# Performance work log

Hardware: AMD Instinct MI355X
Metric: run time of the kernel (lower is better)

## Reference

```python
import math
import jax, jax.numpy as jnp
import numpy as np

L, B, D, Z, H, N = 2048, 8, 1024, 128, 2048, 16
MAXPOS = 2048
LAPLACE_MU, LAPLACE_SIGMA = 0.707107, 0.282095


def setup_inputs() -> dict:
    key = jax.random.key(0)
    ks = jax.random.split(key, 14)
    def rn(k, shp, s=1.0):
        return jax.random.normal(k, shp, dtype=jnp.float32) * s
    return {
        "x": rn(ks[0], (L, B, D)),
        # MultiHeadEMA params (unidirectional: kernel_dim == D)
        "delta": rn(ks[1], (D, N, 1), 0.2),
        "alpha": rn(ks[2], (D, N, 1), 0.2),
        "beta_ema": rn(ks[3], (D, N, 1), 0.02) + 1.0,
        "gamma_ema": rn(ks[4], (D, N)),
        "omega": rn(ks[5], (D,)),
        # projections
        "v_w": rn(ks[6], (D, H), 0.02), "v_b": jnp.zeros((H,), jnp.float32),
        "mx_w": rn(ks[7], (D, Z + H + 2 * D), 0.02),
        "mx_b": jnp.zeros((Z + H + 2 * D,), jnp.float32),
        "h_w": rn(ks[8], (H, D), 0.02), "h_b": jnp.zeros((D,), jnp.float32),
        # q/k affine from shared z
        "qk_gamma": rn(ks[9], (2, Z), 0.1) + 1.0,
        "qk_beta": rn(ks[10], (2, Z), 0.1),
        # simple relative positional bias
        "rel_pos": rn(ks[11], (2 * MAXPOS - 1,), 0.02),
        # prenorm layernorm
        "ln_w": jnp.ones((D,), jnp.float32),
        "ln_b": jnp.zeros((D,), jnp.float32),
    }


def _laplace(x):
    x = (x - LAPLACE_MU) / (LAPLACE_SIGMA * math.sqrt(2.0))
    return 0.5 * (1.0 + jax.lax.erf(x))


def _layer_norm(x, w, b, eps=1e-5):
    mu = jnp.mean(x, axis=-1, keepdims=True)
    var = jnp.mean(jnp.square(x - mu), axis=-1, keepdims=True)
    return (x - mu) * jax.lax.rsqrt(var + eps) * w + b


def _rel_bias(rel_pos, seq_len):
    # SimpleRelativePositionalBias: Toeplitz (L, L) matrix from a 2L-1 vector
    bvec = rel_pos[MAXPOS - seq_len:MAXPOS + seq_len - 1]  # (2L-1,)
    t = jnp.pad(bvec, (0, seq_len))                         # (3L-1,)
    t = jnp.tile(t, seq_len)[:-seq_len].reshape(seq_len, 3 * seq_len - 2)
    r = (2 * seq_len - 1) // 2
    return t[:, r:t.shape[1] - r]                           # (L, L)


def _ema_conv(xn, delta, alpha, beta_ema, gamma_ema, omega, seq_len):
    # xn: (L, B, D) -> silu(EMA(xn) + xn * omega), via FFT convolution
    scale = 1.0 / math.sqrt(N)
    p = jax.nn.sigmoid(delta)                 # (D, N, 1)
    q = 1.0 - p * jax.nn.sigmoid(alpha)       # (D, N, 1)
    vander = jnp.arange(seq_len, dtype=jnp.float32)[None, None, :] * jnp.log(q)  # (D, N, L)
    kernel = jnp.einsum('dnl,dn->dl', p * beta_ema * jnp.exp(vander), gamma_ema * scale)  # (D, L)
    residual = xn * omega                     # (L, B, D)
    xt = jnp.transpose(xn, (1, 2, 0))         # (B, D, L)
    nfft = 2 * seq_len
    kf = jnp.fft.rfft(kernel, n=nfft)         # (D, L+1) complex
    xf = jnp.fft.rfft(xt, n=nfft)             # (B, D, L+1)
    out = jnp.fft.irfft(xf * kf, n=nfft)[..., :seq_len]  # (B, D, L)
    return jax.nn.silu(jnp.transpose(out, (2, 0, 1)) + residual)  # (L, B, D)


def reference(x, delta, alpha, beta_ema, gamma_ema, omega,
              v_w, v_b, mx_w, mx_b, h_w, h_b,
              qk_gamma, qk_beta, rel_pos, ln_w, ln_b):
    seq_len = x.shape[0]
    residual = x
    xn = _layer_norm(x, ln_w, ln_b)                       # prenorm
    v = jax.nn.silu(xn @ v_w + v_b)                        # (L, B, H)
    mx = _ema_conv(xn, delta, alpha, beta_ema, gamma_ema, omega, seq_len)  # (L, B, D)
    base = mx @ mx_w + mx_b                                # (L, B, D+Z+H+D)
    u = jax.nn.sigmoid(base[..., :D])                      # update gate (L, B, D)
    zr = jax.nn.silu(base[..., D:D + Z + H])
    hx = base[..., D + Z + H:]                             # (L, B, D)
    z = zr[..., :Z]                                        # (L, B, Z)
    r = zr[..., Z:]                                        # (L, B, H)
    zqk = z[..., None, :] * qk_gamma + qk_beta             # (L, B, 2, Z)
    q = jnp.transpose(zqk[..., 0, :], (1, 0, 2))           # (B, L, Z)
    k = jnp.transpose(zqk[..., 1, :], (1, 0, 2))           # (B, L, Z)
    vb = jnp.transpose(v, (1, 0, 2))                       # (B, L, H)
    bias = _rel_bias(rel_pos, seq_len)                     # (L, L)
    qk = jnp.einsum('blz,bmz->blm', q, k) / seq_len + bias # (B, L, L)
    attn = _laplace(qk)
    h = jnp.einsum('blm,bmh->blh', attn, vb)               # (B, L, H)
    h = jnp.transpose(h, (1, 0, 2))                        # (L, B, H)
    h = jax.nn.silu(hx + (h * r) @ h_w + h_b)              # (L, B, D)
    out = residual + u * (h - residual)
    return out
```

## Files before the change

kernel.cpp:

```cpp
#include <hip/hip_runtime.h>
#include <hip/hip_bf16.h>
#include <math.h>

typedef unsigned short u16;
typedef unsigned int   u32;
typedef __bf16 bf16x8_t __attribute__((ext_vector_type(8)));
typedef float  f32x4_t  __attribute__((ext_vector_type(4)));

#define DEVI static __device__ __forceinline__

DEVI float bf2f(u16 u){ union{u32 i; float f;} v; v.i = ((u32)u)<<16; return v.f; }
DEVI u16 f2bf(float f){ union{float f; u32 i;} v; v.f = f; u32 i = v.i; i += 0x7fffu + ((i>>16)&1u); return (u16)(i>>16); }
DEVI float sigm(float x){ return 1.0f/(1.0f + __expf(-x)); }
DEVI float silu_(float x){ return x * sigm(x); }

DEVI void gload16(const u16* gsrc, u16* lds){
  __builtin_amdgcn_global_load_lds(
      (const __attribute__((address_space(1))) unsigned int*)gsrc,
      (__attribute__((address_space(3))) unsigned int*)lds, 16, 0, 0);
}

constexpr int L_=2048, B_=8, D_=1024, Z_=128, H_=2048, N_=16;
constexpr int CH_=128, NC_=16;
constexpr int MXN_=4224;

__global__ __launch_bounds__(256) void k_ln(const float* __restrict__ x,
                                            const float* __restrict__ w,
                                            const float* __restrict__ b,
                                            u16* __restrict__ xn){
  int row = blockIdx.x, t = threadIdx.x;
  int l = row >> 3, bb = row & 7;
  const float4* xr = (const float4*)(x + (size_t)row*D_);
  float4 v = xr[t];
  float s  = v.x+v.y+v.z+v.w;
  float sq = v.x*v.x+v.y*v.y+v.z*v.z+v.w*v.w;
  #pragma unroll
  for (int m=1; m<64; m<<=1){ s += __shfl_xor(s, m); sq += __shfl_xor(sq, m); }
  __shared__ float ss[4], sv[4];
  int wv = t>>6;
  if ((t&63)==0){ ss[wv]=s; sv[wv]=sq; }
  __syncthreads();
  s = ss[0]+ss[1]+ss[2]+ss[3]; sq = sv[0]+sv[1]+sv[2]+sv[3];
  float mu = s*(1.0f/D_);
  float var = sq*(1.0f/D_) - mu*mu;
  float rs = rsqrtf(var + 1e-5f);
  float4 wv4 = ((const float4*)w)[t];
  float4 bv4 = ((const float4*)b)[t];
  u16 o0 = f2bf((v.x-mu)*rs*wv4.x+bv4.x);
  u16 o1 = f2bf((v.y-mu)*rs*wv4.y+bv4.y);
  u16 o2 = f2bf((v.z-mu)*rs*wv4.z+bv4.z);
  u16 o3 = f2bf((v.w-mu)*rs*wv4.w+bv4.w);
  *(uint2*)(xn + ((size_t)bb*L_ + l)*D_ + t*4) =
      make_uint2((u32)o0 | ((u32)o1<<16), (u32)o2 | ((u32)o3<<16));
}

__global__ __launch_bounds__(256) void k_tr(const float* __restrict__ in, int R, int C,
                                            u16* __restrict__ out){
  __shared__ u16 TT[32*33];
  int c0 = blockIdx.x*32, r0 = blockIdx.y*32;
  int t = threadIdx.x;
  int lr = t>>3, lc4 = (t&7)*4;
  float4 v = *(const float4*)&in[(size_t)(r0+lr)*C + c0 + lc4];
  TT[(lc4+0)*33 + lr] = f2bf(v.x);
  TT[(lc4+1)*33 + lr] = f2bf(v.y);
  TT[(lc4+2)*33 + lr] = f2bf(v.z);
  TT[(lc4+3)*33 + lr] = f2bf(v.w);
  __syncthreads();
  int orr = t>>3, oc4 = (t&7)*4;
  u16 a0 = TT[orr*33 + oc4+0], a1 = TT[orr*33 + oc4+1];
  u16 a2 = TT[orr*33 + oc4+2], a3 = TT[orr*33 + oc4+3];
  *(uint2*)&out[(size_t)(c0+orr)*R + r0 + oc4] =
      make_uint2((u32)a0 | ((u32)a1<<16), (u32)a2 | ((u32)a3<<16));
}

__global__ void k_ema_params(const float* __restrict__ delta, const float* __restrict__ alpha,
                             const float* __restrict__ beta,  const float* __restrict__ gamma,
                             float* __restrict__ qA, float* __restrict__ wcA, float* __restrict__ qPA){
  int i = blockIdx.x*256 + threadIdx.x;
  if (i >= D_*N_) return;
  float p = 1.0f/(1.0f + expf(-delta[i]));
  float q = 1.0f - p*(1.0f/(1.0f + expf(-alpha[i])));
  qA[i]  = q;
  wcA[i] = p*beta[i]*gamma[i]*0.25f;
  qPA[i] = powf(q, (float)CH_);
}

__global__ __launch_bounds__(256) void k_ema_a(const u16* __restrict__ xn,
                                               const float* __restrict__ qA,
                                               float* __restrict__ F){
  int d = blockIdx.x*256 + threadIdx.x;
  int b = blockIdx.y, c = blockIdx.z;
  float q[N_], s[N_];
  #pragma unroll
  for (int n=0;n<N_;n++){ q[n]=qA[d*N_+n]; s[n]=0.0f; }
  for (int t=0;t<CH_;t++){
    int l = c*CH_ + t;
    float x = bf2f(xn[((size_t)b*L_ + l)*D_ + d]);
    #pragma unroll
    for (int n=0;n<N_;n++) s[n] = q[n]*s[n] + x;
  }
  float* Fo = F + (((size_t)c*B_ + b)*D_ + d)*N_;
  #pragma unroll
  for (int n=0;n<N_;n++) Fo[n] = s[n];
}

__global__ __launch_bounds__(256) void k_ema_b(float* __restrict__ F,
                                               const float* __restrict__ qPA){
  int i = blockIdx.x*256 + threadIdx.x;
  int n = i & (N_-1);
  int d = (i>>4) & (D_-1);
  int b = i >> 14;
  float qP = qPA[d*N_+n];
  float S = 0.0f;
  for (int c=0;c<NC_;c++){
    size_t idx = (((size_t)c*B_ + b)*D_ + d)*N_ + n;
    float f = F[idx];
    F[idx] = S;
    S = qP*S + f;
  }
}

__global__ __launch_bounds__(256) void k_ema_c(const u16* __restrict__ xn,
                                               const float* __restrict__ qA,
                                               const float* __restrict__ wcA,
                                               const float* __restrict__ CY,
                                               const float* __restrict__ omega,
                                               u16* __restrict__ mx){
  int d = blockIdx.x*256 + threadIdx.x;
  int b = blockIdx.y, c = blockIdx.z;
  float q[N_], wc[N_], s[N_];
  const float* cy = CY + (((size_t)c*B_ + b)*D_ + d)*N_;
  #pragma unroll
  for (int n=0;n<N_;n++){ q[n]=qA[d*N_+n]; wc[n]=wcA[d*N_+n]; s[n]=cy[n]; }
  float om = omega[d];
  for (int t=0;t<CH_;t++){
    int l = c*CH_ + t;
    float x = bf2f(xn[((size_t)b*L_ + l)*D_ + d]);
    float acc = 0.0f;
    #pragma unroll
    for (int n=0;n<N_;n++){ s[n] = q[n]*s[n] + x; acc += wc[n]*s[n]; }
    mx[((size_t)b*L_ + l)*D_ + d] = f2bf(silu_(acc + x*om));
  }
}

#define STG(BUF, K0) do {                                                         \
    int _ab = (BUF)*8192;                                                         \
    _Pragma("unroll")                                                             \
    for (int it=0; it<2; ++it){                                                   \
      int idx = it*256 + tid; int r = idx>>2, ch = idx&3;                         \
      gload16(Ab + (size_t)(rowBase + r)*lda + (K0) + ((ch ^ (r&3))*8),           \
              &LDS[_ab + idx*8]);                                                 \
    }                                                                             \
    _Pragma("unroll")                                                             \
    for (int it=0; it<2; ++it){                                                   \
      int idx = it*256 + tid; int r = idx>>2, ch = idx&3;                         \
      gload16(Bb + (size_t)(colBase + r)*ldb + (K0) + ((ch ^ (r&3))*8),           \
              &LDS[_ab + 4096 + idx*8]);                                          \
    }                                                                             \
  } while(0)

#define CMP(BUF) do {                                                             \
    int _ab = (BUF)*8192;                                                         \
    bf16x8_t af[4], bfr[4];                                                       \
    int kfx = (lane4*8) ^ ((lane15&3)<<3);                                        \
    _Pragma("unroll")                                                             \
    for (int m=0;m<4;m++)                                                         \
      af[m]  = *(const bf16x8_t*)&LDS[_ab + (wm + m*16 + lane15)*32 + kfx];       \
    _Pragma("unroll")                                                             \
    for (int n=0;n<4;n++)                                                         \
      bfr[n] = *(const bf16x8_t*)&LDS[_ab + 4096 + (wn + n*16 + lane15)*32 + kfx];\
    __builtin_amdgcn_s_setprio(1);                                                \
    _Pragma("unroll")                                                             \
    for (int m=0;m<4;m++)                                                         \
      _Pragma("unroll")                                                           \
      for (int n=0;n<4;n++)                                                       \
        acc[m][n] = __builtin_amdgcn_mfma_f32_16x16x32_bf16(af[m], bfr[n], acc[m][n], 0,0,0); \
    __builtin_amdgcn_s_setprio(0);                                                \
  } while(0)

template<int OP>
__global__ __launch_bounds__(256) void k_gall(
    const u16* __restrict__ A, int lda, long aStr,
    const u16* __restrict__ Bm, int ldb, long bStr,
    int K,
    u16* __restrict__ C, int ldc, long cStr,
    const float* __restrict__ biasC, const float* __restrict__ biasR,
    const float* __restrict__ relpos,
    const float* __restrict__ qkg, const float* __restrict__ qkb,
    u16* __restrict__ P0, u16* __restrict__ P1,
    u16* __restrict__ P2, u16* __restrict__ P3,
    const u16* __restrict__ RP0, const u16* __restrict__ RP1,
    const float* __restrict__ xin, float* __restrict__ outf, int bb)
{
  __shared__ u16 LDS[16384];
  int zz = blockIdx.z;
  const u16* Ab = A + (size_t)zz*aStr;
  const u16* Bb = Bm + (size_t)zz*bStr;

  int gx = gridDim.x;
  int f = blockIdx.x + gx*blockIdx.y;
  int q8 = (gx*gridDim.y) >> 3;
  int wg = (f & 7)*q8 + (f >> 3);
  int rowBase = (wg / gx)*128;
  int colBase = (wg % gx)*128;

  int tid = threadIdx.x;
  int lane = tid & 63, wave = tid >> 6;
  int wm = (wave>>1)*64, wn = (wave&1)*64;
  int lane15 = lane & 15, lane4 = lane >> 4;

  f32x4_t acc[4][4];
  #pragma unroll
  for (int m=0;m<4;m++)
    #pragma unroll
    for (int n=0;n<4;n++) acc[m][n] = (f32x4_t){0.f,0.f,0.f,0.f};

  int nt = K >> 5;
  STG(0, 0);
  STG(1, 32);
  for (int t = 0; t < nt; ++t){
    if (t + 1 < nt) { asm volatile("s_waitcnt vmcnt(4)" ::: "memory"); }
    else            { asm volatile("s_waitcnt vmcnt(0)" ::: "memory"); }
    __builtin_amdgcn_s_barrier();
    __builtin_amdgcn_sched_barrier(0);
    CMP(t & 1);
    if (t + 2 < nt) {
      __builtin_amdgcn_s_barrier();
      STG(t & 1, (t+2)*32);
    }
  }

  u16* Cb  = C  ? C  + (size_t)zz*cStr : nullptr;
  u16* P0b = P0 ? P0 + (size_t)zz*((size_t)L_*D_) : nullptr;
  u16* P1b = P1 ? P1 + (size_t)zz*((size_t)L_*D_) : nullptr;
  u16* P2b = P2 ? P2 + (size_t)zz*((size_t)L_*Z_) : nullptr;
  u16* P3b = P3 ? P3 + (size_t)zz*((size_t)L_*Z_) : nullptr;
  const u16* RP0b = RP0 ? RP0 + (size_t)zz*(OP==3 ? (size_t)L_*H_ : (size_t)L_*D_) : nullptr;
  const u16* RP1b = RP1 ? RP1 + (size_t)zz*((size_t)L_*D_) : nullptr;
  int bglob = bb + zz;

  #pragma unroll
  for (int m=0;m<4;m++) {
    #pragma unroll
    for (int n=0;n<4;n++) {
      int col = colBase + wn + n*16 + lane15;
      #pragma unroll
      for (int r2=0;r2<4;r2++) {
        int row = rowBase + wm + m*16 + lane4*4 + r2;
        float v = acc[m][n][r2];
        if (OP == 0) {
          Cb[(size_t)row*ldc + col] = f2bf(silu_(v + biasR[row]));
        } else if (OP == 1) {
          v += biasC[col];
          if (col < 1024) {
            P0b[(size_t)row*1024 + col] = f2bf(sigm(v));
          } else if (col < 1152) {
            float s = silu_(v);
            int zi = col - 1024;
            P2b[(size_t)row*128 + zi] = f2bf(s*qkg[zi]     + qkb[zi]);
            P3b[(size_t)row*128 + zi] = f2bf(s*qkg[128+zi] + qkb[128+zi]);
          } else if (col < 3200) {
            Cb[(size_t)row*2048 + (col-1152)] = f2bf(silu_(v));
          } else {
            P1b[(size_t)row*1024 + (col-3200)] = f2bf(v);
          }
        } else if (OP == 2) {
          v = v*(1.0f/(float)L_) + relpos[2047 + col - row];
          v = 0.5f*(1.0f + erff((v - 0.707107f)*2.5066282746f));
          Cb[(size_t)row*ldc + col] = f2bf(v);
        } else if (OP == 3) {
          v *= bf2f(RP0b[(size_t)row*ldc + col]);
          Cb[(size_t)row*ldc + col] = f2bf(v);
        } else {
          v += biasC[col];
          float hx = bf2f(RP0b[(size_t)row*1024 + col]);
          float hval = silu_(hx + v);
          size_t gi = ((size_t)row*B_ + bglob)*D_ + col;
          float xv = xin[gi];
          float uu = bf2f(RP1b[(size_t)row*1024 + col]);
          outf[gi] = xv + uu*(hval - xv);
        }
      }
    }
  }
}

extern "C" void kernel_launch(void* const* d_in, const int* in_sizes, int n_in,
                              void* d_out, int out_size, void* d_ws, size_t ws_size,
                              hipStream_t stream) {
  const float* x      = (const float*)d_in[0];
  const float* delta  = (const float*)d_in[1];
  const float* alpha  = (const float*)d_in[2];
  const float* betaE  = (const float*)d_in[3];
  const float* gammaE = (const float*)d_in[4];
  const float* omega  = (const float*)d_in[5];
  const float* v_w    = (const float*)d_in[6];
  const float* v_b    = (const float*)d_in[7];
  const float* mx_w   = (const float*)d_in[8];
  const float* mx_b   = (const float*)d_in[9];
  const float* h_w    = (const float*)d_in[10];
  const float* h_b    = (const float*)d_in[11];
  const float* qkg    = (const float*)d_in[12];
  const float* qkb    = (const float*)d_in[13];
  const float* relpos = (const float*)d_in[14];
  const float* ln_w   = (const float*)d_in[15];
  const float* ln_b   = (const float*)d_in[16];
  float* out = (float*)d_out;

  const size_t fixedB = 92733440ull;
  const size_t perNB  = 42991616ull;
  int NB = 8;
  while (NB > 1 && fixedB + (size_t)NB*perNB > ws_size) NB >>= 1;
  int NG = B_ / NB;

  char* ws = (char*)d_ws;
  size_t o = 0;
  auto alloc = [&](size_t sz){ size_t r = o; o += sz; return r; };
  u16* XN    = (u16*)(ws + alloc(33554432));
  u16* MX    = (u16*)(ws + alloc(33554432));
  u16* VWT   = (u16*)(ws + alloc(4194304));
  u16* MXWT  = (u16*)(ws + alloc((size_t)MXN_*D_*2));
  u16* HWT   = (u16*)(ws + alloc(4194304));
  float* EQ  = (float*)(ws + alloc(65536));
  float* EW  = (float*)(ws + alloc(65536));
  float* EP  = (float*)(ws + alloc(65536));
  float* Ff  = (float*)(ws + alloc(8388608));
  u16* VT    = (u16*)(ws + alloc((size_t)NB*8388608));
  u16* ATTN  = (u16*)(ws + alloc((size_t)NB*8388608));
  u16* Rb    = (u16*)(ws + alloc((size_t)NB*8388608));
  u16* HRb   = (u16*)(ws + alloc((size_t)NB*8388608));
  u16* Ub    = (u16*)(ws + alloc((size_t)NB*4194304));
  u16* HXb   = (u16*)(ws + alloc((size_t)NB*4194304));
  u16* Qb    = (u16*)(ws + alloc((size_t)NB*524288));
  u16* Kb    = (u16*)(ws + alloc((size_t)NB*524288));

  k_ln<<<L_*B_, 256, 0, stream>>>(x, ln_w, ln_b, XN);
  k_ema_params<<<(D_*N_+255)/256, 256, 0, stream>>>(delta, alpha, betaE, gammaE, EQ, EW, EP);
  k_ema_a<<<dim3(D_/256, B_, NC_), 256, 0, stream>>>(XN, EQ, Ff);
  k_ema_b<<<(B_*D_*N_)/256, 256, 0, stream>>>(Ff, EP);
  k_ema_c<<<dim3(D_/256, B_, NC_), 256, 0, stream>>>(XN, EQ, EW, Ff, omega, MX);
  k_tr<<<dim3(H_/32, D_/32), 256, 0, stream>>>(v_w, D_, H_, VWT);
  k_tr<<<dim3(MXN_/32, D_/32), 256, 0, stream>>>(mx_w, D_, MXN_, MXWT);
  k_tr<<<dim3(D_/32, H_/32), 256, 0, stream>>>(h_w, H_, D_, HWT);

  for (int g = 0; g < NG; ++g) {
    int b0 = g*NB;
    k_gall<0><<<dim3(L_/128, H_/128, NB), 256, 0, stream>>>(
        VWT, D_, 0L, XN + (size_t)b0*L_*D_, D_, (long)L_*D_, D_,
        VT, L_, (long)H_*L_,
        nullptr, v_b, nullptr, nullptr, nullptr,
        nullptr, nullptr, nullptr, nullptr,
        nullptr, nullptr, nullptr, nullptr, 0);
    k_gall<1><<<dim3(MXN_/128, L_/128, NB), 256, 0, stream>>>(
        MX + (size_t)b0*L_*D_, D_, (long)L_*D_, MXWT, D_, 0L, D_,
        Rb, H_, (long)L_*H_,
        mx_b, nullptr, nullptr, qkg, qkb,
        Ub, HXb, Qb, Kb,
        nullptr, nullptr, nullptr, nullptr, 0);
    k_gall<2><<<dim3(L_/128, L_/128, NB), 256, 0, stream>>>(
        Qb, Z_, (long)L_*Z_, Kb, Z_, (long)L_*Z_, Z_,
        ATTN, L_, (long)L_*L_,
        nullptr, nullptr, relpos, nullptr, nullptr,
        nullptr, nullptr, nullptr, nullptr,
        nullptr, nullptr, nullptr, nullptr, 0);
    k_gall<3><<<dim3(H_/128, L_/128, NB), 256, 0, stream>>>(
        ATTN, L_, (long)L_*L_, VT, L_, (long)H_*L_, L_,
        HRb, H_, (long)L_*H_,
        nullptr, nullptr, nullptr, nullptr, nullptr,
        nullptr, nullptr, nullptr, nullptr,
        Rb, nullptr, nullptr, nullptr, 0);
    k_gall<4><<<dim3(D_/128, L_/128, NB), 256, 0, stream>>>(
        HRb, H_, (long)L_*H_, HWT, H_, 0L, H_,
        nullptr, 0, 0L,
        h_b, nullptr, nullptr, nullptr, nullptr,
        nullptr, nullptr, nullptr, nullptr,
        HXb, Ub, x, out, b0);
  }
}
```

Baseline: 831.9 us.

## Triple-buffer GEMM LDS stages with single barrier and new XOR swizzle layout

```diff
diff --git a/kernel.cpp b/kernel.cpp
--- a/kernel.cpp
+++ b/kernel.cpp
@@ -147,14 +147,18 @@
     int _ab = (BUF)*8192;                                                         \
     _Pragma("unroll")                                                             \
     for (int it=0; it<2; ++it){                                                   \
-      int idx = it*256 + tid; int r = idx>>2, ch = idx&3;                         \
-      gload16(Ab + (size_t)(rowBase + r)*lda + (K0) + ((ch ^ (r&3))*8),           \
+      int idx = it*256 + tid;                                                     \
+      int s = (idx&7) ^ ((idx>>3)&7);                                             \
+      int r = (idx>>3) + ((s>>2)<<6);                                             \
+      gload16(Ab + (size_t)(rowBase + r)*lda + (K0) + ((s&3)*8),                  \
               &LDS[_ab + idx*8]);                                                 \
     }                                                                             \
     _Pragma("unroll")                                                             \
     for (int it=0; it<2; ++it){                                                   \
-      int idx = it*256 + tid; int r = idx>>2, ch = idx&3;                         \
-      gload16(Bb + (size_t)(colBase + r)*ldb + (K0) + ((ch ^ (r&3))*8),           \
+      int idx = it*256 + tid;                                                     \
+      int s = (idx&7) ^ ((idx>>3)&7);                                             \
+      int r = (idx>>3) + ((s>>2)<<6);                                             \
+      gload16(Bb + (size_t)(colBase + r)*ldb + (K0) + ((s&3)*8),                  \
               &LDS[_ab + 4096 + idx*8]);                                          \
     }                                                                             \
   } while(0)
@@ -162,13 +166,14 @@
 #define CMP(BUF) do {                                                             \
     int _ab = (BUF)*8192;                                                         \
     bf16x8_t af[4], bfr[4];                                                       \
-    int kfx = (lane4*8) ^ ((lane15&3)<<3);                                        \
     _Pragma("unroll")                                                             \
     for (int m=0;m<4;m++)                                                         \
-      af[m]  = *(const bf16x8_t*)&LDS[_ab + (wm + m*16 + lane15)*32 + kfx];       \
+      af[m]  = *(const bf16x8_t*)&LDS[_ab + (m*16 + lane15)*64 +                  \
+                                      ((((lane4 + ah4) ^ l7))<<3)];               \
     _Pragma("unroll")                                                             \
     for (int n=0;n<4;n++)                                                         \
-      bfr[n] = *(const bf16x8_t*)&LDS[_ab + 4096 + (wn + n*16 + lane15)*32 + kfx];\
+      bfr[n] = *(const bf16x8_t*)&LDS[_ab + 4096 + (n*16 + lane15)*64 +           \
+                                      ((((lane4 + bh4) ^ l7))<<3)];               \
     __builtin_amdgcn_s_setprio(1);                                                \
     _Pragma("unroll")                                                             \
     for (int m=0;m<4;m++)                                                         \
@@ -192,7 +197,7 @@
     const u16* __restrict__ RP0, const u16* __restrict__ RP1,
     const float* __restrict__ xin, float* __restrict__ outf, int bb)
 {
-  __shared__ u16 LDS[16384];
+  __shared__ u16 LDS[24576];
   int zz = blockIdx.z;
   const u16* Ab = A + (size_t)zz*aStr;
   const u16* Bb = Bm + (size_t)zz*bStr;
@@ -208,6 +213,9 @@
   int lane = tid & 63, wave = tid >> 6;
   int wm = (wave>>1)*64, wn = (wave&1)*64;
   int lane15 = lane & 15, lane4 = lane >> 4;
+  int ah4 = wm >> 4;
+  int bh4 = wn >> 4;
+  int l7  = lane15 & 7;
 
   f32x4_t acc[4][4];
   #pragma unroll
@@ -223,11 +231,9 @@
     else            { asm volatile("s_waitcnt vmcnt(0)" ::: "memory"); }
     __builtin_amdgcn_s_barrier();
     __builtin_amdgcn_sched_barrier(0);
-    CMP(t & 1);
-    if (t + 2 < nt) {
-      __builtin_amdgcn_s_barrier();
-      STG(t & 1, (t+2)*32);
-    }
+    int cb = t % 3;
+    if (t + 2 < nt) { int nb = (t+2) % 3; STG(nb, (t+2)*32); }
+    CMP(cb);
   }
 
   u16* Cb  = C  ? C  + (size_t)zz*cStr : nullptr;
```

Result: no change. 829.0 us (-0.3%).
